# Optimization experiments

Measured on AMD Instinct MI355X. Metric: run time of the kernel, lower is better.

The kernel has to match this reference:

```python
import jax, jax.numpy as jnp
import numpy as np

B, IN, H = 64, 1024, 1024

def _lin(x, W, b):
    # torch nn.Linear: y = x @ W.T + b, W:[out,in]
    return x @ W.T + b

def setup_inputs() -> dict:
    key = jax.random.key(0)
    ks = jax.random.split(key, 16)
    s_in = 1.0 / np.sqrt(IN)
    s_cat = 1.0 / np.sqrt(IN + H)
    s_h = 1.0 / np.sqrt(H)
    return {
        "x": jax.random.normal(ks[0], (B, IN), jnp.float32),
        "h": jax.random.normal(ks[1], (B, H), jnp.float32),
        "C": jax.random.normal(ks[2], (B, H, H), jnp.float32) * 0.02,
        "Wq": jax.random.normal(ks[3], (H, IN), jnp.float32) * s_in,
        "bq": jax.random.normal(ks[4], (H,), jnp.float32) * s_in,
        "Wk": jax.random.normal(ks[5], (H, IN), jnp.float32) * s_in,
        "bk": jax.random.normal(ks[6], (H,), jnp.float32) * s_in,
        "Wv": jax.random.normal(ks[7], (H, IN), jnp.float32) * s_in,
        "bv": jax.random.normal(ks[8], (H,), jnp.float32) * s_in,
        "Wf": jax.random.normal(ks[9], (H, IN + H), jnp.float32) * s_cat,
        "bf": jax.random.normal(ks[10], (H,), jnp.float32) * s_cat,
        "Wi": jax.random.normal(ks[11], (H, IN + H), jnp.float32) * s_cat,
        "bi": jax.random.normal(ks[12], (H,), jnp.float32) * s_cat,
        "Wo": jax.random.normal(ks[13], (H, H), jnp.float32) * s_h,
        "bo": jax.random.normal(ks[14], (H,), jnp.float32) * s_h,
    }

def reference(x, h, C, Wq, bq, Wk, bk, Wv, bv, Wf, bf, Wi, bi, Wo, bo):
    q = _lin(x, Wq, bq)            # [B,H]
    k = _lin(x, Wk, bk)            # [B,H]
    v = _lin(x, Wv, bv)            # [B,H]
    combined = jnp.concatenate([x, h], axis=-1)       # [B,IN+H]
    f = jax.nn.sigmoid(_lin(combined, Wf, bf))        # [B,H]
    i = jax.nn.sigmoid(_lin(combined, Wi, bi))        # [B,H]
    # gated matrix-memory update: C_new[b,m,n] = f[b,m]*C[b,m,n] + i[b,m]*k[b,m]*v[b,n]
    C_new = f[:, :, None] * C + (i * k)[:, :, None] * v[:, None, :]
    # readout: matvec with q then tanh and output projection
    r = jnp.einsum('bmn,bn->bm', C_new, q)            # [B,H]
    h_new = _lin(jnp.tanh(r), Wo, bo)                 # [B,H]
    return (h_new, C_new)
```

## Files before the change

kernel.cpp:

```cpp
#include <hip/hip_runtime.h>
#include <math.h>

#define HB 64
#define HD 1024
#define KS 128
#define XS 68

typedef float f32x4 __attribute__((ext_vector_type(4)));

__device__ __forceinline__ void splitk_tile(
    const float* __restrict__ X0, int noff,
    const float* __restrict__ W, int K,
    int m0, int k0,
    float* __restrict__ P)
{
    __shared__ __align__(16) float Xs[32][XS];
    __shared__ __align__(16) float Ws[32][XS];
    const int t  = threadIdx.x;
    const int bx = t & 15;
    const int my = t >> 4;
    float acc[4][4] = {};

    for (int kc = 0; kc < KS; kc += 32) {
        const int n0 = k0 + kc;
        #pragma unroll
        for (int i = 0; i < 2; ++i) {
            int u = t + 256 * i;
            int b = u >> 3, nq = u & 7;
            float4 xv = *(const float4*)&X0[b * HD + (n0 - noff) + nq * 4];
            Xs[nq * 4 + 0][b] = xv.x; Xs[nq * 4 + 1][b] = xv.y;
            Xs[nq * 4 + 2][b] = xv.z; Xs[nq * 4 + 3][b] = xv.w;
        }
        #pragma unroll
        for (int i = 0; i < 2; ++i) {
            int u = t + 256 * i;
            int mm = u >> 3, nq = u & 7;
            float4 wv = *(const float4*)&W[(long long)(m0 + mm) * K + n0 + nq * 4];
            Ws[nq * 4 + 0][mm] = wv.x; Ws[nq * 4 + 1][mm] = wv.y;
            Ws[nq * 4 + 2][mm] = wv.z; Ws[nq * 4 + 3][mm] = wv.w;
        }
        __syncthreads();
        #pragma unroll
        for (int n = 0; n < 32; ++n) {
            float4 xv = *(const float4*)&Xs[n][bx * 4];
            float4 wv = *(const float4*)&Ws[n][my * 4];
            float xe[4] = {xv.x, xv.y, xv.z, xv.w};
            float we[4] = {wv.x, wv.y, wv.z, wv.w};
            #pragma unroll
            for (int i = 0; i < 4; ++i)
                #pragma unroll
                for (int j = 0; j < 4; ++j)
                    acc[i][j] = fmaf(xe[i], we[j], acc[i][j]);
        }
        __syncthreads();
    }
    #pragma unroll
    for (int i = 0; i < 4; ++i)
        #pragma unroll
        for (int j = 0; j < 4; ++j)
            P[(bx * 4 + i) * HD + m0 + my * 4 + j] = acc[i][j];
}

__global__ __launch_bounds__(256) void qkvfi_splitk(
    const float* __restrict__ x, const float* __restrict__ h,
    const float* __restrict__ Wq, const float* __restrict__ Wk,
    const float* __restrict__ Wv, const float* __restrict__ Wf,
    const float* __restrict__ Wi, float* __restrict__ P)
{
    const int gy = blockIdx.y;
    const float* W; int K, split;
    if (gy < 24) {
        int g = gy >> 3; split = gy & 7; K = HD;
        W = (g == 0) ? Wq : (g == 1) ? Wk : Wv;
    } else {
        int tt = gy - 24; int g = tt >> 4; split = tt & 15; K = 2 * HD;
        W = g ? Wi : Wf;
    }
    const int k0 = split * KS;
    const float* X0; int noff;
    if (k0 < HD) { X0 = x; noff = 0; } else { X0 = h; noff = HD; }
    splitk_tile(X0, noff, W, K, blockIdx.x * 64, k0, P + (size_t)gy * (HB * HD));
}

__global__ __launch_bounds__(256) void out_splitk(
    const float* __restrict__ tr, const float* __restrict__ Wo,
    float* __restrict__ P2)
{
    const int split = blockIdx.y;
    splitk_tile(tr, 0, Wo, HD, blockIdx.x * 64, split * KS,
                P2 + (size_t)split * (HB * HD));
}

__global__ __launch_bounds__(256) void reduce_qkvfi(
    const float* __restrict__ P,
    const float* __restrict__ bq, const float* __restrict__ bk,
    const float* __restrict__ bv, const float* __restrict__ bfv,
    const float* __restrict__ biv,
    float* __restrict__ q, float* __restrict__ k, float* __restrict__ v,
    float* __restrict__ fg, float* __restrict__ ig)
{
    const int o = blockIdx.x * 256 + threadIdx.x;
    const int g = o >> 16;
    const int rem = o & 65535;
    const int m = rem & (HD - 1);
    int base, ns, act; const float* bias; float* out;
    switch (g) {
        case 0:  base = 0;  ns = 8;  bias = bq;  out = q;  act = 0; break;
        case 1:  base = 8;  ns = 8;  bias = bk;  out = k;  act = 0; break;
        case 2:  base = 16; ns = 8;  bias = bv;  out = v;  act = 0; break;
        case 3:  base = 24; ns = 16; bias = bfv; out = fg; act = 1; break;
        default: base = 40; ns = 16; bias = biv; out = ig; act = 1; break;
    }
    float s = bias[m];
    for (int i = 0; i < ns; ++i) s += P[(size_t)(base + i) * 65536 + rem];
    if (act) s = 1.0f / (1.0f + expf(-s));
    out[rem] = s;
}

__global__ __launch_bounds__(256) void reduce_out(
    const float* __restrict__ P2, const float* __restrict__ bo,
    float* __restrict__ hnew)
{
    const int o = blockIdx.x * 256 + threadIdx.x;
    const int m = o & (HD - 1);
    float s = bo[m];
    #pragma unroll
    for (int i = 0; i < 8; ++i) s += P2[(size_t)i * 65536 + o];
    hnew[o] = s;
}

__global__ __launch_bounds__(256) void update_kernel(
    const float* __restrict__ C,
    const float* __restrict__ q, const float* __restrict__ k,
    const float* __restrict__ v, const float* __restrict__ fg,
    const float* __restrict__ ig,
    float* __restrict__ Cn, float* __restrict__ tr)
{
    const int wid  = threadIdx.x >> 6;
    const int lane = threadIdx.x & 63;
    const int row  = blockIdx.x * 4 + wid;
    const int b    = row >> 10;
    const int m    = row & (HD - 1);

    const float fm  = fg[b * HD + m];
    const float ikm = ig[b * HD + m] * k[b * HD + m];

    const f32x4* C4 = (const f32x4*)C;
    const float4* V4 = (const float4*)v;
    const float4* Q4 = (const float4*)q;
    f32x4*       N4 = (f32x4*)Cn;

    const int base  = row * (HD / 4);
    const int vbase = b * (HD / 4);

    float racc = 0.f;
    #pragma unroll
    for (int j = 0; j < 4; ++j) {
        int o = lane + 64 * j;
        f32x4 c4 = __builtin_nontemporal_load(&C4[base + o]);
        float4 v4 = V4[vbase + o];
        float4 q4 = Q4[vbase + o];
        f32x4 cn;
        cn.x = fmaf(fm, c4.x, ikm * v4.x);
        cn.y = fmaf(fm, c4.y, ikm * v4.y);
        cn.z = fmaf(fm, c4.z, ikm * v4.z);
        cn.w = fmaf(fm, c4.w, ikm * v4.w);
        __builtin_nontemporal_store(cn, &N4[base + o]);
        racc += cn.x * q4.x + cn.y * q4.y + cn.z * q4.z + cn.w * q4.w;
    }
    #pragma unroll
    for (int off = 32; off; off >>= 1) racc += __shfl_xor(racc, off);
    if (lane == 0) tr[row] = tanhf(racc);
}

extern "C" void kernel_launch(void* const* d_in, const int* in_sizes, int n_in,
                              void* d_out, int out_size, void* d_ws, size_t ws_size,
                              hipStream_t stream) {
    const float* x  = (const float*)d_in[0];
    const float* h  = (const float*)d_in[1];
    const float* C  = (const float*)d_in[2];
    const float* Wq = (const float*)d_in[3];
    const float* bq = (const float*)d_in[4];
    const float* Wk = (const float*)d_in[5];
    const float* bk = (const float*)d_in[6];
    const float* Wv = (const float*)d_in[7];
    const float* bv = (const float*)d_in[8];
    const float* Wf = (const float*)d_in[9];
    const float* bf = (const float*)d_in[10];
    const float* Wi = (const float*)d_in[11];
    const float* bi = (const float*)d_in[12];
    const float* Wo = (const float*)d_in[13];
    const float* bo = (const float*)d_in[14];

    float* outp = (float*)d_out;
    float* hnew = outp;
    float* Cn   = outp + HB * HD;

    const size_t SL = (size_t)HB * HD;
    float* ws = (float*)d_ws;
    float* q  = ws + 0 * SL;
    float* k  = ws + 1 * SL;
    float* v  = ws + 2 * SL;
    float* fg = ws + 3 * SL;
    float* ig = ws + 4 * SL;
    float* tr = ws + 5 * SL;
    float* P  = ws + 6 * SL;
    float* P2 = ws + 62 * SL;

    qkvfi_splitk<<<dim3(16, 56), 256, 0, stream>>>(x, h, Wq, Wk, Wv, Wf, Wi, P);
    reduce_qkvfi<<<dim3(1280), 256, 0, stream>>>(P, bq, bk, bv, bf, bi,
                                                 q, k, v, fg, ig);
    update_kernel<<<dim3((HB * HD) / 4), 256, 0, stream>>>(
        C, q, k, v, fg, ig, Cn, tr);
    out_splitk<<<dim3(16, 8), 256, 0, stream>>>(tr, Wo, P2);
    reduce_out<<<dim3(256), 256, 0, stream>>>(P2, bo, hnew);
}
```

Baseline: 128.7 us.

## Prefetch split-K tiles in registers, vectorize reductions, two rows per wave

The split-K GEMM tile now loads the next 32-wide K chunk into registers while it computes on the current shared-memory tile. It also swaps the thread mapping so each thread writes its partial results as float4 stores. Both reduction kernels are vectorized to float4 and launch a quarter as many blocks. The update kernel now handles two C rows per wave, so the v/q loads are reused and twice the memory is in flight. These changes target memory latency and instruction count, at the cost of more register pressure.

```diff
diff --git a/kernel.cpp b/kernel.cpp
--- a/kernel.cpp
+++ b/kernel.cpp
@@ -17,29 +17,40 @@
     __shared__ __align__(16) float Xs[32][XS];
     __shared__ __align__(16) float Ws[32][XS];
     const int t  = threadIdx.x;
-    const int bx = t & 15;
-    const int my = t >> 4;
+    const int bx = t >> 4;
+    const int my = t & 15;
     float acc[4][4] = {};
 
+    float4 xp[2], wp[2];
+    #pragma unroll
+    for (int i = 0; i < 2; ++i) {
+        int u = t + 256 * i;
+        int r = u >> 3, nq = u & 7;
+        xp[i] = *(const float4*)&X0[r * HD + (k0 - noff) + nq * 4];
+        wp[i] = *(const float4*)&W[(long long)(m0 + r) * K + k0 + nq * 4];
+    }
+
     for (int kc = 0; kc < KS; kc += 32) {
-        const int n0 = k0 + kc;
         #pragma unroll
         for (int i = 0; i < 2; ++i) {
             int u = t + 256 * i;
-            int b = u >> 3, nq = u & 7;
-            float4 xv = *(const float4*)&X0[b * HD + (n0 - noff) + nq * 4];
-            Xs[nq * 4 + 0][b] = xv.x; Xs[nq * 4 + 1][b] = xv.y;
-            Xs[nq * 4 + 2][b] = xv.z; Xs[nq * 4 + 3][b] = xv.w;
-        }
-        #pragma unroll
-        for (int i = 0; i < 2; ++i) {
-            int u = t + 256 * i;
-            int mm = u >> 3, nq = u & 7;
-            float4 wv = *(const float4*)&W[(long long)(m0 + mm) * K + n0 + nq * 4];
-            Ws[nq * 4 + 0][mm] = wv.x; Ws[nq * 4 + 1][mm] = wv.y;
-            Ws[nq * 4 + 2][mm] = wv.z; Ws[nq * 4 + 3][mm] = wv.w;
+            int r = u >> 3, nq = u & 7;
+            Xs[nq * 4 + 0][r] = xp[i].x; Xs[nq * 4 + 1][r] = xp[i].y;
+            Xs[nq * 4 + 2][r] = xp[i].z; Xs[nq * 4 + 3][r] = xp[i].w;
+            Ws[nq * 4 + 0][r] = wp[i].x; Ws[nq * 4 + 1][r] = wp[i].y;
+            Ws[nq * 4 + 2][r] = wp[i].z; Ws[nq * 4 + 3][r] = wp[i].w;
         }
         __syncthreads();
+        if (kc + 32 < KS) {
+            const int n0 = k0 + kc + 32;
+            #pragma unroll
+            for (int i = 0; i < 2; ++i) {
+                int u = t + 256 * i;
+                int r = u >> 3, nq = u & 7;
+                xp[i] = *(const float4*)&X0[r * HD + (n0 - noff) + nq * 4];
+                wp[i] = *(const float4*)&W[(long long)(m0 + r) * K + n0 + nq * 4];
+            }
+        }
         #pragma unroll
         for (int n = 0; n < 32; ++n) {
             float4 xv = *(const float4*)&Xs[n][bx * 4];
@@ -55,10 +66,10 @@
         __syncthreads();
     }
     #pragma unroll
-    for (int i = 0; i < 4; ++i)
-        #pragma unroll
-        for (int j = 0; j < 4; ++j)
-            P[(bx * 4 + i) * HD + m0 + my * 4 + j] = acc[i][j];
+    for (int i = 0; i < 4; ++i) {
+        float4 o4 = make_float4(acc[i][0], acc[i][1], acc[i][2], acc[i][3]);
+        *(float4*)&P[(bx * 4 + i) * HD + m0 + my * 4] = o4;
+    }
 }
 
 __global__ __launch_bounds__(256) void qkvfi_splitk(
@@ -99,10 +110,10 @@
     float* __restrict__ q, float* __restrict__ k, float* __restrict__ v,
     float* __restrict__ fg, float* __restrict__ ig)
 {
-    const int o = blockIdx.x * 256 + threadIdx.x;
-    const int g = o >> 16;
-    const int rem = o & 65535;
-    const int m = rem & (HD - 1);
+    const int o4 = blockIdx.x * 256 + threadIdx.x;
+    const int g  = o4 >> 14;
+    const int r4 = o4 & 16383;
+    const int m4 = r4 & 255;
     int base, ns, act; const float* bias; float* out;
     switch (g) {
         case 0:  base = 0;  ns = 8;  bias = bq;  out = q;  act = 0; break;
@@ -111,22 +122,33 @@
         case 3:  base = 24; ns = 16; bias = bfv; out = fg; act = 1; break;
         default: base = 40; ns = 16; bias = biv; out = ig; act = 1; break;
     }
-    float s = bias[m];
-    for (int i = 0; i < ns; ++i) s += P[(size_t)(base + i) * 65536 + rem];
-    if (act) s = 1.0f / (1.0f + expf(-s));
-    out[rem] = s;
+    float4 s = ((const float4*)bias)[m4];
+    const float4* P4 = (const float4*)P;
+    for (int i = 0; i < ns; ++i) {
+        float4 p = P4[(size_t)(base + i) * 16384 + r4];
+        s.x += p.x; s.y += p.y; s.z += p.z; s.w += p.w;
+    }
+    if (act) {
+        s.x = 1.0f / (1.0f + expf(-s.x)); s.y = 1.0f / (1.0f + expf(-s.y));
+        s.z = 1.0f / (1.0f + expf(-s.z)); s.w = 1.0f / (1.0f + expf(-s.w));
+    }
+    ((float4*)out)[r4] = s;
 }
 
 __global__ __launch_bounds__(256) void reduce_out(
     const float* __restrict__ P2, const float* __restrict__ bo,
     float* __restrict__ hnew)
 {
-    const int o = blockIdx.x * 256 + threadIdx.x;
-    const int m = o & (HD - 1);
-    float s = bo[m];
-    #pragma unroll
-    for (int i = 0; i < 8; ++i) s += P2[(size_t)i * 65536 + o];
-    hnew[o] = s;
+    const int o4 = blockIdx.x * 256 + threadIdx.x;
+    const int m4 = o4 & 255;
+    float4 s = ((const float4*)bo)[m4];
+    const float4* P4 = (const float4*)P2;
+    #pragma unroll
+    for (int i = 0; i < 8; ++i) {
+        float4 p = P4[(size_t)i * 16384 + o4];
+        s.x += p.x; s.y += p.y; s.z += p.z; s.w += p.w;
+    }
+    ((float4*)hnew)[o4] = s;
 }
 
 __global__ __launch_bounds__(256) void update_kernel(
@@ -138,39 +160,52 @@
 {
     const int wid  = threadIdx.x >> 6;
     const int lane = threadIdx.x & 63;
-    const int row  = blockIdx.x * 4 + wid;
-    const int b    = row >> 10;
-    const int m    = row & (HD - 1);
-
-    const float fm  = fg[b * HD + m];
-    const float ikm = ig[b * HD + m] * k[b * HD + m];
-
-    const f32x4* C4 = (const f32x4*)C;
+    const int pair = blockIdx.x * 4 + wid;
+    const int row0 = pair * 2;
+    const int b    = row0 >> 10;
+    const int m0   = row0 & (HD - 1);
+
+    const float f0  = fg[b * HD + m0];
+    const float f1  = fg[b * HD + m0 + 1];
+    const float ik0 = ig[b * HD + m0] * k[b * HD + m0];
+    const float ik1 = ig[b * HD + m0 + 1] * k[b * HD + m0 + 1];
+
+    const f32x4*  C4 = (const f32x4*)C;
     const float4* V4 = (const float4*)v;
     const float4* Q4 = (const float4*)q;
-    f32x4*       N4 = (f32x4*)Cn;
-
-    const int base  = row * (HD / 4);
+    f32x4*        N4 = (f32x4*)Cn;
+
+    const int base0 = row0 * (HD / 4);
+    const int base1 = base0 + (HD / 4);
     const int vbase = b * (HD / 4);
 
-    float racc = 0.f;
+    float r0 = 0.f, r1 = 0.f;
     #pragma unroll
     for (int j = 0; j < 4; ++j) {
         int o = lane + 64 * j;
-        f32x4 c4 = __builtin_nontemporal_load(&C4[base + o]);
+        f32x4 c0 = __builtin_nontemporal_load(&C4[base0 + o]);
+        f32x4 c1 = __builtin_nontemporal_load(&C4[base1 + o]);
         float4 v4 = V4[vbase + o];
         float4 q4 = Q4[vbase + o];
-        f32x4 cn;
-        cn.x = fmaf(fm, c4.x, ikm * v4.x);
-        cn.y = fmaf(fm, c4.y, ikm * v4.y);
-        cn.z = fmaf(fm, c4.z, ikm * v4.z);
-        cn.w = fmaf(fm, c4.w, ikm * v4.w);
-        __builtin_nontemporal_store(cn, &N4[base + o]);
-        racc += cn.x * q4.x + cn.y * q4.y + cn.z * q4.z + cn.w * q4.w;
-    }
-    #pragma unroll
-    for (int off = 32; off; off >>= 1) racc += __shfl_xor(racc, off);
-    if (lane == 0) tr[row] = tanhf(racc);
+        f32x4 n0, n1;
+        n0.x = fmaf(f0, c0.x, ik0 * v4.x); n0.y = fmaf(f0, c0.y, ik0 * v4.y);
+        n0.z = fmaf(f0, c0.z, ik0 * v4.z); n0.w = fmaf(f0, c0.w, ik0 * v4.w);
+        n1.x = fmaf(f1, c1.x, ik1 * v4.x); n1.y = fmaf(f1, c1.y, ik1 * v4.y);
+        n1.z = fmaf(f1, c1.z, ik1 * v4.z); n1.w = fmaf(f1, c1.w, ik1 * v4.w);
+        __builtin_nontemporal_store(n0, &N4[base0 + o]);
+        __builtin_nontemporal_store(n1, &N4[base1 + o]);
+        r0 += n0.x * q4.x + n0.y * q4.y + n0.z * q4.z + n0.w * q4.w;
+        r1 += n1.x * q4.x + n1.y * q4.y + n1.z * q4.z + n1.w * q4.w;
+    }
+    #pragma unroll
+    for (int off = 32; off; off >>= 1) {
+        r0 += __shfl_xor(r0, off);
+        r1 += __shfl_xor(r1, off);
+    }
+    if (lane == 0) {
+        tr[row0]     = tanhf(r0);
+        tr[row0 + 1] = tanhf(r1);
+    }
 }
 
 extern "C" void kernel_launch(void* const* d_in, const int* in_sizes, int n_in,
@@ -208,10 +243,10 @@
     float* P2 = ws + 62 * SL;
 
     qkvfi_splitk<<<dim3(16, 56), 256, 0, stream>>>(x, h, Wq, Wk, Wv, Wf, Wi, P);
-    reduce_qkvfi<<<dim3(1280), 256, 0, stream>>>(P, bq, bk, bv, bf, bi,
-                                                 q, k, v, fg, ig);
-    update_kernel<<<dim3((HB * HD) / 4), 256, 0, stream>>>(
+    reduce_qkvfi<<<dim3(320), 256, 0, stream>>>(P, bq, bk, bv, bf, bi,
+                                                q, k, v, fg, ig);
+    update_kernel<<<dim3((HB * HD) / 8), 256, 0, stream>>>(
         C, q, k, v, fg, ig, Cn, tr);
     out_splitk<<<dim3(16, 8), 256, 0, stream>>>(tr, Wo, P2);
-    reduce_out<<<dim3(256), 256, 0, stream>>>(P2, bo, hnew);
-}
+    reduce_out<<<dim3(64), 256, 0, stream>>>(P2, bo, hnew);
+}
```

New measurement: 129.6 us. About the same (+0.7%).
